# Kernel optimization log

Hardware: AMD Instinct MI355X
Metric: run time of the kernel (lower is better)

Reference implementation:

```python
import jax, jax.numpy as jnp
import numpy as np
from jax import lax

B, H, W, C = 4, 96, 96, 256
F = 256
KH = KW = 3
K = KH * KW
DG = 1
CG = C // DG
SH = SW = 1
DH = DW = 1
PAD_T = (DH * (KH - 1)) // 2  # 'same' padding (top/left) for 3x3 dil 1
PAD_L = (DW * (KW - 1)) // 2


def setup_inputs() -> dict:
    key = jax.random.key(0)
    k1, k2, k3 = jax.random.split(key, 3)
    x = jax.random.normal(k1, (B, H, W, C), jnp.float32)
    # offset/mask conv weights (orig init zeros; small random to exercise sampling)
    om_kernel = jax.random.normal(k2, (KH, KW, C, DG * 3 * K), jnp.float32) * 0.01
    om_bias = jnp.zeros((DG * 3 * K,), jnp.float32)
    stdv = 1.0 / np.sqrt(C * KH * KW)
    kernel = jax.random.uniform(k3, (K * C, F), jnp.float32, -stdv, stdv)
    bias = jnp.zeros((F,), jnp.float32)
    return {"x": x, "om_kernel": om_kernel, "om_bias": om_bias, "kernel": kernel, "bias": bias}


def reference(x, om_kernel, om_bias, kernel, bias):
    Bx, Hx, Wx, Cx = x.shape
    # offset/mask prediction conv (NHWC, 'SAME', matches keras Conv2D)
    om = lax.conv_general_dilated(
        x, om_kernel, (SH, SW), "SAME", rhs_dilation=(DH, DW),
        dimension_numbers=("NHWC", "HWIO", "NHWC")) + om_bias
    Ho, Wo = om.shape[1], om.shape[2]
    off = om[..., : 2 * DG * K].reshape(Bx, Ho, Wo, DG, K, 2)  # (dy, dx) per group/kpoint
    mask = jax.nn.sigmoid(om[..., 2 * DG * K :]).reshape(Bx, Ho, Wo, DG, K) * 2.0

    # base sampling grid: y = ho*SH - PAD_T + ki*DH (+ dy), similarly x
    base_y = (jnp.arange(Ho) * SH - PAD_T)[:, None] + (jnp.arange(KH) * DH)[None, :]  # [Ho,KH]
    base_x = (jnp.arange(Wo) * SW - PAD_L)[:, None] + (jnp.arange(KW) * DW)[None, :]  # [Wo,KW]
    gy = jnp.broadcast_to(base_y[:, None, :, None], (Ho, Wo, KH, KW)).reshape(Ho, Wo, K)
    gx = jnp.broadcast_to(base_x[None, :, None, :], (Ho, Wo, KH, KW)).reshape(Ho, Wo, K)

    py = gy[None, :, :, None, :].astype(x.dtype) + off[..., 0]  # [B,Ho,Wo,DG,K]
    px = gx[None, :, :, None, :].astype(x.dtype) + off[..., 1]

    # reorder to [B, N, DG] with N = Ho*Wo*K (K varies fastest after spatial)
    N = Ho * Wo * K
    py = py.transpose(0, 1, 2, 4, 3).reshape(Bx, N, DG)
    px = px.transpose(0, 1, 2, 4, 3).reshape(Bx, N, DG)
    mask_t = mask.transpose(0, 1, 2, 4, 3).reshape(Bx, N, DG)

    y0 = jnp.floor(py)
    x0 = jnp.floor(px)
    fy = py - y0
    fx = px - x0

    xf = x.reshape(Bx, Hx * Wx, DG, CG)
    val = jnp.zeros((Bx, N, DG, CG), x.dtype)
    for yi, wy in ((y0, 1.0 - fy), (y0 + 1.0, fy)):
        for xi, wx in ((x0, 1.0 - fx), (x0 + 1.0, fx)):
            valid = (yi >= 0) & (yi < Hx) & (xi >= 0) & (xi < Wx)
            yc = jnp.clip(yi, 0, Hx - 1).astype(jnp.int32)
            xc = jnp.clip(xi, 0, Wx - 1).astype(jnp.int32)
            lin = yc * Wx + xc  # [B,N,DG]
            g = jnp.take_along_axis(xf, lin[..., None], axis=1)  # [B,N,DG,CG]
            val = val + g * (wy * wx * valid.astype(x.dtype))[..., None]

    # modulate and im2col -> GEMM
    cols = (val * mask_t[..., None]).reshape(Bx, Ho * Wo, K * Cx)
    out = jnp.matmul(cols, kernel).reshape(Bx, Ho, Wo, -1) + bias
    return out
```

## Files before the change

### kernel.cpp

```cpp
#include <hip/hip_runtime.h>
#include <hip/hip_bf16.h>
#include <stdint.h>
#include <stddef.h>


namespace {
constexpr int H  = 96, W = 96, C = 256, F = 256;
constexpr int HP = 98;
constexpr int NP = 4 * 96 * 96;
constexpr int KC = 9 * 256;
}

typedef __attribute__((ext_vector_type(8))) short bf16x8;
typedef __attribute__((ext_vector_type(4))) float floatx4;

__device__ __forceinline__ void load_lds16(const void* g, void* l) {
  __builtin_amdgcn_global_load_lds((const __attribute__((address_space(1))) void*)g,
                                   (__attribute__((address_space(3))) void*)l,
                                   16, 0, 0);
}

__device__ __forceinline__ unsigned short bf16bits(float f) {
  __hip_bfloat16 h = __float2bfloat16(f);
  return *reinterpret_cast<unsigned short*>(&h);
}

__global__ __launch_bounds__(256) void k_pad(const float* __restrict__ x,
                                             uint2* __restrict__ xp) {
  const int tid = threadIdx.x;
  const int sub = tid >> 6, c4 = tid & 63;
  const int pp  = blockIdx.x * 4 + sub;
  const int b   = pp / (HP * HP);
  const int r   = pp % (HP * HP);
  const int y   = r / HP, xq = r % HP;
  uint2 o = {0u, 0u};
  if (y >= 1 && y <= H && xq >= 1 && xq <= W) {
    const float4 v = *(const float4*)(x + ((size_t)((b * H + (y - 1)) * W + (xq - 1))) * C + c4 * 4);
    o.x = (uint32_t)bf16bits(v.x) | ((uint32_t)bf16bits(v.y) << 16);
    o.y = (uint32_t)bf16bits(v.z) | ((uint32_t)bf16bits(v.w) << 16);
  }
  xp[(size_t)pp * 64 + c4] = o;
}

__global__ __launch_bounds__(256) void k_omw(const float* __restrict__ omk,
                                             __hip_bfloat16* __restrict__ wom) {
  const int kk = blockIdx.x;
  const int oc = blockIdx.y;
  const int c  = threadIdx.x;
  float v = (oc < 27) ? omk[(size_t)(kk * 256 + c) * 27 + oc] : 0.f;
  wom[(size_t)oc * KC + kk * 256 + c] = __float2bfloat16(v);
}

__global__ __launch_bounds__(256) void k_wt(const float* __restrict__ kern,
                                            __hip_bfloat16* __restrict__ wt) {
  __shared__ float t[64][65];
  const int kc0 = blockIdx.x * 64, f0 = blockIdx.y * 64;
  const int rr = threadIdx.x >> 6, cc = threadIdx.x & 63;
#pragma unroll
  for (int i = 0; i < 16; ++i) {
    const int row = rr * 16 + i;
    t[row][cc] = kern[(size_t)(kc0 + row) * F + f0 + cc];
  }
  __syncthreads();
#pragma unroll
  for (int i = 0; i < 16; ++i) {
    const int frow = rr * 16 + i;
    wt[(size_t)(f0 + frow) * KC + kc0 + cc] = __float2bfloat16(t[cc][frow]);
  }
}

__global__ __launch_bounds__(256) void k_omgemm(const __hip_bfloat16* __restrict__ xp,
                                                const __hip_bfloat16* __restrict__ wom,
                                                float* __restrict__ pOm) {
  __shared__ __align__(16) char lds[10240];
  const int tid  = threadIdx.x;
  const int m0   = blockIdx.x * 128;
  const int s    = blockIdx.y;
  const int lane = tid & 63, wave = tid >> 6;
  const int quad = lane >> 4, l16 = lane & 15;

  const int kp = tid & 3;
  const __hip_bfloat16* abase[2];
#pragma unroll
  for (int j = 0; j < 2; ++j) {
    const int row = (tid >> 2) + j * 64;
    const int p = m0 + row;
    const int b = p / (H * W);
    const int hw = p % (H * W);
    const int h = hw / W, w = hw % W;
    abase[j] = (const __hip_bfloat16*)xp + ((size_t)(b * HP + h) * HP + w) * C + kp * 8;
  }
  const __hip_bfloat16* bbase = wom + (size_t)(tid >> 2) * KC + kp * 8;

  floatx4 acc[2][2];
#pragma unroll
  for (int i = 0; i < 2; ++i)
#pragma unroll
    for (int j = 0; j < 2; ++j) acc[i][j] = (floatx4){0.f, 0.f, 0.f, 0.f};

  const int kbeg = s * 384;
#pragma unroll 1
  for (int k0 = kbeg; k0 < kbeg + 384; k0 += 32) {
    const int kk = k0 >> 8;
    const int c0 = k0 & 255;
    const int kh = kk / 3, kw = kk % 3;
    const int aoff = (kh * HP + kw) * C + c0;

    __syncthreads();
    load_lds16(abase[0] + aoff, &lds[tid * 16]);
    load_lds16(abase[1] + aoff, &lds[4096 + tid * 16]);
    if (tid < 128) load_lds16(bbase + k0, &lds[8192 + tid * 16]);
    __syncthreads();

    bf16x8 af[2], bfr[2];
#pragma unroll
    for (int mt = 0; mt < 2; ++mt)
      af[mt] = *(const bf16x8*)&lds[((wave * 32 + mt * 16 + l16) * 32 + quad * 8) * 2];
#pragma unroll
    for (int nt = 0; nt < 2; ++nt)
      bfr[nt] = *(const bf16x8*)&lds[8192 + ((nt * 16 + l16) * 32 + quad * 8) * 2];
#pragma unroll
    for (int mt = 0; mt < 2; ++mt)
#pragma unroll
      for (int nt = 0; nt < 2; ++nt)
        acc[mt][nt] = __builtin_amdgcn_mfma_f32_16x16x32_bf16(af[mt], bfr[nt], acc[mt][nt], 0, 0, 0);
  }

#pragma unroll
  for (int mt = 0; mt < 2; ++mt)
#pragma unroll
    for (int nt = 0; nt < 2; ++nt) {
      const int gm = m0 + wave * 32 + mt * 16 + quad * 4;
      const int gn = nt * 16 + l16;
#pragma unroll
      for (int r = 0; r < 4; ++r)
        __hip_atomic_fetch_add(&pOm[(size_t)(gm + r) * 32 + gn], acc[mt][nt][r],
                               __ATOMIC_RELAXED, __HIP_MEMORY_SCOPE_AGENT);
    }
}

__global__ __launch_bounds__(256) void k_sample(const uint2* __restrict__ xp,
                                                const float* __restrict__ pOm,
                                                const float* __restrict__ om_bias,
                                                uint2* __restrict__ cols) {
  const int tid = threadIdx.x;
  const int sub = tid >> 6, cid = tid & 63;
  const int p   = blockIdx.x * 4 + sub;
  const int b   = p / (H * W);
  const int hw  = p % (H * W);
  const int h = hw / W, w = hw % W;

  __shared__ float s_py[4][9], s_px[4][9], s_m[4][9];
  if (cid < 9) {
    const int k = cid;
    const float dy = om_bias[2 * k]     + pOm[(size_t)p * 32 + 2 * k];
    const float dx = om_bias[2 * k + 1] + pOm[(size_t)p * 32 + 2 * k + 1];
    const float mv = om_bias[18 + k]    + pOm[(size_t)p * 32 + 18 + k];
    s_py[sub][k] = (float)(h - 1 + k / 3) + dy;
    s_px[sub][k] = (float)(w - 1 + k % 3) + dx;
    s_m[sub][k]  = 2.f / (1.f + __expf(-mv));
  }
  __syncthreads();

  const uint2* __restrict__ xb = xp + (size_t)b * (HP * HP * 64) + cid;
  uint2* __restrict__ ob = cols + (size_t)p * (KC / 4) + cid;

#pragma unroll 1
  for (int k = 0; k < 9; ++k) {
    const float py = s_py[sub][k], px = s_px[sub][k], m = s_m[sub][k];
    const float y0f = floorf(py), x0f = floorf(px);
    const float fy = py - y0f, fx = px - x0f;
    const int y0 = (int)y0f, x0 = (int)x0f;
    float v0 = 0.f, v1 = 0.f, v2 = 0.f, v3 = 0.f;
#pragma unroll
    for (int dy2 = 0; dy2 < 2; ++dy2) {
#pragma unroll
      for (int dx2 = 0; dx2 < 2; ++dx2) {
        const int yi = y0 + dy2, xi = x0 + dx2;
        const bool valid = (yi >= 0) & (yi < H) & (xi >= 0) & (xi < W);
        const float wgt = valid ? (dy2 ? fy : 1.f - fy) * (dx2 ? fx : 1.f - fx) : 0.f;
        const int yc = min(max(yi + 1, 0), HP - 1);
        const int xc = min(max(xi + 1, 0), HP - 1);
        const uint2 v = xb[(size_t)(yc * HP + xc) * 64];
        v0 += wgt * __uint_as_float(v.x << 16);
        v1 += wgt * __uint_as_float(v.x & 0xffff0000u);
        v2 += wgt * __uint_as_float(v.y << 16);
        v3 += wgt * __uint_as_float(v.y & 0xffff0000u);
      }
    }
    uint2 o;
    o.x = (uint32_t)bf16bits(v0 * m) | ((uint32_t)bf16bits(v1 * m) << 16);
    o.y = (uint32_t)bf16bits(v2 * m) | ((uint32_t)bf16bits(v3 * m) << 16);
    ob[k * 64] = o;
  }
}

__global__ __launch_bounds__(256) void k_gemm(const __hip_bfloat16* __restrict__ A,
                                              const __hip_bfloat16* __restrict__ Bt,
                                              const float* __restrict__ bias,
                                              float* __restrict__ out) {
  __shared__ __align__(16) char lds[14336];

  const int tid  = threadIdx.x;
  const int m0   = blockIdx.x * 96;
  const int n0   = blockIdx.y * 128;
  const int lane = tid & 63, wave = tid >> 6;
  const int wm = wave & 1, wn = wave >> 1;
  const int quad = lane >> 4, l16 = lane & 15;

  floatx4 acc[3][4];
#pragma unroll
  for (int i = 0; i < 3; ++i)
#pragma unroll
    for (int j = 0; j < 4; ++j) acc[i][j] = (floatx4){0.f, 0.f, 0.f, 0.f};

#pragma unroll 1
  for (int k0 = 0; k0 < KC; k0 += 32) {
    __syncthreads();
    {
      const int row = tid >> 2, kp = tid & 3;
      load_lds16(A + (size_t)(m0 + row) * KC + k0 + kp * 8, &lds[tid * 16]);
      if (tid < 128)
        load_lds16(A + (size_t)(m0 + 64 + row) * KC + k0 + kp * 8, &lds[4096 + tid * 16]);
      load_lds16(Bt + (size_t)(n0 + row) * KC + k0 + kp * 8, &lds[6144 + tid * 16]);
      load_lds16(Bt + (size_t)(n0 + 64 + row) * KC + k0 + kp * 8, &lds[10240 + tid * 16]);
    }
    __syncthreads();

    bf16x8 af[3], bfr[4];
#pragma unroll
    for (int mt = 0; mt < 3; ++mt)
      af[mt] = *(const bf16x8*)&lds[((wm * 48 + mt * 16 + l16) * 32 + quad * 8) * 2];
#pragma unroll
    for (int nt = 0; nt < 4; ++nt)
      bfr[nt] = *(const bf16x8*)&lds[6144 + ((wn * 64 + nt * 16 + l16) * 32 + quad * 8) * 2];
#pragma unroll
    for (int mt = 0; mt < 3; ++mt)
#pragma unroll
      for (int nt = 0; nt < 4; ++nt)
        acc[mt][nt] = __builtin_amdgcn_mfma_f32_16x16x32_bf16(af[mt], bfr[nt], acc[mt][nt], 0, 0, 0);
  }

#pragma unroll
  for (int mt = 0; mt < 3; ++mt) {
#pragma unroll
    for (int nt = 0; nt < 4; ++nt) {
      const int gm = m0 + wm * 48 + mt * 16 + quad * 4;
      const int gn = n0 + wn * 64 + nt * 16 + l16;
      const float bs = bias[gn];
#pragma unroll
      for (int r = 0; r < 4; ++r)
        out[(size_t)(gm + r) * F + gn] = acc[mt][nt][r] + bs;
    }
  }
}

extern "C" void kernel_launch(void* const* d_in, const int* in_sizes, int n_in,
                              void* d_out, int out_size, void* d_ws, size_t ws_size,
                              hipStream_t stream) {
  const float* x    = (const float*)d_in[0];
  const float* omk  = (const float*)d_in[1];
  const float* omb  = (const float*)d_in[2];
  const float* kern = (const float*)d_in[3];
  const float* bias = (const float*)d_in[4];
  float* out = (float*)d_out;

  char* ws = (char*)d_ws;
  size_t off = 0;
  __hip_bfloat16* wt   = (__hip_bfloat16*)(ws + off); off += (size_t)F * KC * 2;
  __hip_bfloat16* xp   = (__hip_bfloat16*)(ws + off); off += (size_t)4 * HP * HP * C * 2;
  __hip_bfloat16* wom  = (__hip_bfloat16*)(ws + off); off += (size_t)32 * KC * 2;
  float*          pOm  = (float*)(ws + off);          off += (size_t)NP * 32 * 4;
  __hip_bfloat16* cols = (__hip_bfloat16*)(ws + off);

  k_pad   <<<dim3(4 * HP * HP / 4), 256, 0, stream>>>(x, (uint2*)xp);
  k_omw   <<<dim3(9, 32),           256, 0, stream>>>(omk, wom);
  k_wt    <<<dim3(KC / 64, F / 64), 256, 0, stream>>>(kern, wt);
  hipMemsetAsync(pOm, 0, (size_t)NP * 32 * 4, stream);
  k_omgemm<<<dim3(NP / 128, 6),     256, 0, stream>>>(xp, wom, pOm);
  k_sample<<<dim3(NP / 4),          256, 0, stream>>>((const uint2*)xp, pOm, omb, (uint2*)cols);
  k_gemm  <<<dim3(NP / 96, F / 128), 256, 0, stream>>>(cols, wt, bias, out);
}
```

Baseline: 250.5 us.

## Fuse deformable bilinear sampling into the GEMM A-tile load

Merges the sampling kernel and the GEMM into one kernel. Each block precomputes the per-pixel, per-kernel-point corner offsets and mask-scaled bilinear weights in LDS, then builds the bf16 A tile on the fly from the padded input for every K step. This removes the write and re-read of the large im2col cols buffer and one launch. In exchange, sampling is repeated for each of the two N-tile blocks, the gathers sit on the GEMM's critical path with no overlap, and the larger LDS footprint plus launch_bounds(256,3) may limit occupancy.

```diff
diff --git a/kernel.cpp b/kernel.cpp
--- a/kernel.cpp
+++ b/kernel.cpp
@@ -139,74 +139,52 @@
     }
 }
 
-__global__ __launch_bounds__(256) void k_sample(const uint2* __restrict__ xp,
-                                                const float* __restrict__ pOm,
-                                                const float* __restrict__ om_bias,
-                                                uint2* __restrict__ cols) {
-  const int tid = threadIdx.x;
-  const int sub = tid >> 6, cid = tid & 63;
-  const int p   = blockIdx.x * 4 + sub;
-  const int b   = p / (H * W);
-  const int hw  = p % (H * W);
-  const int h = hw / W, w = hw % W;
-
-  __shared__ float s_py[4][9], s_px[4][9], s_m[4][9];
-  if (cid < 9) {
-    const int k = cid;
+__global__ __launch_bounds__(256, 3) void k_fused(const uint2* __restrict__ xpu,
+                                                  const float* __restrict__ pOm,
+                                                  const float* __restrict__ om_bias,
+                                                  const __hip_bfloat16* __restrict__ Bt,
+                                                  const float* __restrict__ bias,
+                                                  float* __restrict__ out) {
+  __shared__ __align__(16) char s_a[6144];
+  __shared__ __align__(16) char s_b[8192];
+  __shared__ __align__(16) float s_ow[96 * 9 * 8];
+
+  const int tid  = threadIdx.x;
+  const int m0   = blockIdx.x * 96;
+  const int n0   = blockIdx.y * 128;
+  const int b    = m0 / (H * W);
+  const int h    = (m0 % (H * W)) / W;
+  const int lane = tid & 63, wave = tid >> 6;
+  const int wm = wave & 1, wn = wave >> 1;
+  const int quad = lane >> 4, l16 = lane & 15;
+
+#pragma unroll 1
+  for (int i = tid; i < 96 * 9; i += 256) {
+    const int wq = i % 96, k = i / 96;
+    const int p  = m0 + wq;
     const float dy = om_bias[2 * k]     + pOm[(size_t)p * 32 + 2 * k];
     const float dx = om_bias[2 * k + 1] + pOm[(size_t)p * 32 + 2 * k + 1];
     const float mv = om_bias[18 + k]    + pOm[(size_t)p * 32 + 18 + k];
-    s_py[sub][k] = (float)(h - 1 + k / 3) + dy;
-    s_px[sub][k] = (float)(w - 1 + k % 3) + dx;
-    s_m[sub][k]  = 2.f / (1.f + __expf(-mv));
-  }
-  __syncthreads();
-
-  const uint2* __restrict__ xb = xp + (size_t)b * (HP * HP * 64) + cid;
-  uint2* __restrict__ ob = cols + (size_t)p * (KC / 4) + cid;
-
-#pragma unroll 1
-  for (int k = 0; k < 9; ++k) {
-    const float py = s_py[sub][k], px = s_px[sub][k], m = s_m[sub][k];
-    const float y0f = floorf(py), x0f = floorf(px);
-    const float fy = py - y0f, fx = px - x0f;
+    const float m  = 2.f / (1.f + __expf(-mv));
+    const float sy = (float)(h - 1 + k / 3) + dy;
+    const float sx = (float)(wq - 1 + k % 3) + dx;
+    const float y0f = floorf(sy), x0f = floorf(sx);
+    const float fy = sy - y0f, fx = sx - x0f;
     const int y0 = (int)y0f, x0 = (int)x0f;
-    float v0 = 0.f, v1 = 0.f, v2 = 0.f, v3 = 0.f;
-#pragma unroll
-    for (int dy2 = 0; dy2 < 2; ++dy2) {
-#pragma unroll
-      for (int dx2 = 0; dx2 < 2; ++dx2) {
-        const int yi = y0 + dy2, xi = x0 + dx2;
-        const bool valid = (yi >= 0) & (yi < H) & (xi >= 0) & (xi < W);
-        const float wgt = valid ? (dy2 ? fy : 1.f - fy) * (dx2 ? fx : 1.f - fx) : 0.f;
-        const int yc = min(max(yi + 1, 0), HP - 1);
-        const int xc = min(max(xi + 1, 0), HP - 1);
-        const uint2 v = xb[(size_t)(yc * HP + xc) * 64];
-        v0 += wgt * __uint_as_float(v.x << 16);
-        v1 += wgt * __uint_as_float(v.x & 0xffff0000u);
-        v2 += wgt * __uint_as_float(v.y << 16);
-        v3 += wgt * __uint_as_float(v.y & 0xffff0000u);
-      }
-    }
-    uint2 o;
-    o.x = (uint32_t)bf16bits(v0 * m) | ((uint32_t)bf16bits(v1 * m) << 16);
-    o.y = (uint32_t)bf16bits(v2 * m) | ((uint32_t)bf16bits(v3 * m) << 16);
-    ob[k * 64] = o;
-  }
-}
-
-__global__ __launch_bounds__(256) void k_gemm(const __hip_bfloat16* __restrict__ A,
-                                              const __hip_bfloat16* __restrict__ Bt,
-                                              const float* __restrict__ bias,
-                                              float* __restrict__ out) {
-  __shared__ __align__(16) char lds[14336];
-
-  const int tid  = threadIdx.x;
-  const int m0   = blockIdx.x * 96;
-  const int n0   = blockIdx.y * 128;
-  const int lane = tid & 63, wave = tid >> 6;
-  const int wm = wave & 1, wn = wave >> 1;
-  const int quad = lane >> 4, l16 = lane & 15;
+    float* ow = &s_ow[(size_t)(wq * 9 + k) * 8];
+#pragma unroll
+    for (int c2 = 0; c2 < 4; ++c2) {
+      const int dy2 = c2 >> 1, dx2 = c2 & 1;
+      const int yi = y0 + dy2, xi = x0 + dx2;
+      const bool valid = (yi >= 0) & (yi < H) & (xi >= 0) & (xi < W);
+      const float wgt = valid ? (dy2 ? fy : 1.f - fy) * (dx2 ? fx : 1.f - fx) * m : 0.f;
+      const int yc = min(max(yi + 1, 0), HP - 1);
+      const int xc = min(max(xi + 1, 0), HP - 1);
+      const int off = ((b * HP + yc) * HP + xc) * 64;
+      ow[c2 * 2]     = __int_as_float(off);
+      ow[c2 * 2 + 1] = wgt;
+    }
+  }
 
   floatx4 acc[3][4];
 #pragma unroll
@@ -216,24 +194,60 @@
 
 #pragma unroll 1
   for (int k0 = 0; k0 < KC; k0 += 32) {
+    const int kk = k0 >> 8;
+    const int cb = (k0 & 255) >> 2;
+
     __syncthreads();
     {
       const int row = tid >> 2, kp = tid & 3;
-      load_lds16(A + (size_t)(m0 + row) * KC + k0 + kp * 8, &lds[tid * 16]);
-      if (tid < 128)
-        load_lds16(A + (size_t)(m0 + 64 + row) * KC + k0 + kp * 8, &lds[4096 + tid * 16]);
-      load_lds16(Bt + (size_t)(n0 + row) * KC + k0 + kp * 8, &lds[6144 + tid * 16]);
-      load_lds16(Bt + (size_t)(n0 + 64 + row) * KC + k0 + kp * 8, &lds[10240 + tid * 16]);
+      load_lds16(Bt + (size_t)(n0 + row)      * KC + k0 + kp * 8, &s_b[tid * 16]);
+      load_lds16(Bt + (size_t)(n0 + 64 + row) * KC + k0 + kp * 8, &s_b[4096 + tid * 16]);
+    }
+#pragma unroll
+    for (int u = 0; u < 3; ++u) {
+      const int id  = tid + u * 256;
+      const int pxl = id >> 3, g = id & 7;
+      const float4* owp = (const float4*)&s_ow[(size_t)(pxl * 9 + kk) * 8];
+      const float4 ow0 = owp[0], ow1 = owp[1];
+      float v0 = 0.f, v1 = 0.f, v2 = 0.f, v3 = 0.f;
+      {
+        const uint2 v = xpu[(size_t)__float_as_int(ow0.x) + cb + g];
+        const float wg = ow0.y;
+        v0 += wg * __uint_as_float(v.x << 16); v1 += wg * __uint_as_float(v.x & 0xffff0000u);
+        v2 += wg * __uint_as_float(v.y << 16); v3 += wg * __uint_as_float(v.y & 0xffff0000u);
+      }
+      {
+        const uint2 v = xpu[(size_t)__float_as_int(ow0.z) + cb + g];
+        const float wg = ow0.w;
+        v0 += wg * __uint_as_float(v.x << 16); v1 += wg * __uint_as_float(v.x & 0xffff0000u);
+        v2 += wg * __uint_as_float(v.y << 16); v3 += wg * __uint_as_float(v.y & 0xffff0000u);
+      }
+      {
+        const uint2 v = xpu[(size_t)__float_as_int(ow1.x) + cb + g];
+        const float wg = ow1.y;
+        v0 += wg * __uint_as_float(v.x << 16); v1 += wg * __uint_as_float(v.x & 0xffff0000u);
+        v2 += wg * __uint_as_float(v.y << 16); v3 += wg * __uint_as_float(v.y & 0xffff0000u);
+      }
+      {
+        const uint2 v = xpu[(size_t)__float_as_int(ow1.z) + cb + g];
+        const float wg = ow1.w;
+        v0 += wg * __uint_as_float(v.x << 16); v1 += wg * __uint_as_float(v.x & 0xffff0000u);
+        v2 += wg * __uint_as_float(v.y << 16); v3 += wg * __uint_as_float(v.y & 0xffff0000u);
+      }
+      uint2 o;
+      o.x = (uint32_t)bf16bits(v0) | ((uint32_t)bf16bits(v1) << 16);
+      o.y = (uint32_t)bf16bits(v2) | ((uint32_t)bf16bits(v3) << 16);
+      *(uint2*)&s_a[pxl * 64 + g * 8] = o;
     }
     __syncthreads();
 
     bf16x8 af[3], bfr[4];
 #pragma unroll
     for (int mt = 0; mt < 3; ++mt)
-      af[mt] = *(const bf16x8*)&lds[((wm * 48 + mt * 16 + l16) * 32 + quad * 8) * 2];
+      af[mt] = *(const bf16x8*)&s_a[((wm * 48 + mt * 16 + l16) * 32 + quad * 8) * 2];
 #pragma unroll
     for (int nt = 0; nt < 4; ++nt)
-      bfr[nt] = *(const bf16x8*)&lds[6144 + ((wn * 64 + nt * 16 + l16) * 32 + quad * 8) * 2];
+      bfr[nt] = *(const bf16x8*)&s_b[((wn * 64 + nt * 16 + l16) * 32 + quad * 8) * 2];
 #pragma unroll
     for (int mt = 0; mt < 3; ++mt)
 #pragma unroll
@@ -271,13 +285,11 @@
   __hip_bfloat16* xp   = (__hip_bfloat16*)(ws + off); off += (size_t)4 * HP * HP * C * 2;
   __hip_bfloat16* wom  = (__hip_bfloat16*)(ws + off); off += (size_t)32 * KC * 2;
   float*          pOm  = (float*)(ws + off);          off += (size_t)NP * 32 * 4;
-  __hip_bfloat16* cols = (__hip_bfloat16*)(ws + off);
 
   k_pad   <<<dim3(4 * HP * HP / 4), 256, 0, stream>>>(x, (uint2*)xp);
   k_omw   <<<dim3(9, 32),           256, 0, stream>>>(omk, wom);
   k_wt    <<<dim3(KC / 64, F / 64), 256, 0, stream>>>(kern, wt);
   hipMemsetAsync(pOm, 0, (size_t)NP * 32 * 4, stream);
   k_omgemm<<<dim3(NP / 128, 6),     256, 0, stream>>>(xp, wom, pOm);
-  k_sample<<<dim3(NP / 4),          256, 0, stream>>>((const uint2*)xp, pOm, omb, (uint2*)cols);
-  k_gemm  <<<dim3(NP / 96, F / 128), 256, 0, stream>>>(cols, wt, bias, out);
-}
+  k_fused <<<dim3(NP / 96, F / 128), 256, 0, stream>>>((const uint2*)xp, pOm, omb, wt, bias, out);
+}
```

Measured after the change: 283.7 us. 1.13x slower.

## Merge prep kernels and memset into one launch; widen sampling to 16-byte loads

Applied to the files above, without the earlier changes.

Pad/convert, offset-weight conversion, main-weight transpose and the pOm zeroing are folded into one k_prep kernel that branches on block index, replacing three launches plus a memset. The sampling kernel now handles 8 pixels per block with 32 threads each doing 16-byte (8 bf16) loads and stores. Per-tap bilinear offsets and mask-folded weights are precomputed once into shared memory instead of being recomputed per thread. This cuts launch overhead and per-thread address arithmetic, at the cost of branch-divergent block roles in the fused prep kernel.

```diff
diff --git a/kernel.cpp b/kernel.cpp
--- a/kernel.cpp
+++ b/kernel.cpp
@@ -9,6 +9,11 @@
 constexpr int HP = 98;
 constexpr int NP = 4 * 96 * 96;
 constexpr int KC = 9 * 256;
+
+constexpr int NB_PAD  = 4 * HP * HP / 8;
+constexpr int NB_OMW  = 9 * 32;
+constexpr int NB_WT   = (KC / 64) * (F / 64);
+constexpr int NB_ZERO = NP * 32 * 4 / 4096;
 }
 
 typedef __attribute__((ext_vector_type(8))) short bf16x8;
@@ -20,52 +25,64 @@
                                    16, 0, 0);
 }
 
-__device__ __forceinline__ unsigned short bf16bits(float f) {
-  __hip_bfloat16 h = __float2bfloat16(f);
-  return *reinterpret_cast<unsigned short*>(&h);
-}
-
-__global__ __launch_bounds__(256) void k_pad(const float* __restrict__ x,
-                                             uint2* __restrict__ xp) {
-  const int tid = threadIdx.x;
-  const int sub = tid >> 6, c4 = tid & 63;
-  const int pp  = blockIdx.x * 4 + sub;
-  const int b   = pp / (HP * HP);
-  const int r   = pp % (HP * HP);
-  const int y   = r / HP, xq = r % HP;
-  uint2 o = {0u, 0u};
-  if (y >= 1 && y <= H && xq >= 1 && xq <= W) {
-    const float4 v = *(const float4*)(x + ((size_t)((b * H + (y - 1)) * W + (xq - 1))) * C + c4 * 4);
-    o.x = (uint32_t)bf16bits(v.x) | ((uint32_t)bf16bits(v.y) << 16);
-    o.y = (uint32_t)bf16bits(v.z) | ((uint32_t)bf16bits(v.w) << 16);
-  }
-  xp[(size_t)pp * 64 + c4] = o;
-}
-
-__global__ __launch_bounds__(256) void k_omw(const float* __restrict__ omk,
-                                             __hip_bfloat16* __restrict__ wom) {
-  const int kk = blockIdx.x;
-  const int oc = blockIdx.y;
-  const int c  = threadIdx.x;
-  float v = (oc < 27) ? omk[(size_t)(kk * 256 + c) * 27 + oc] : 0.f;
-  wom[(size_t)oc * KC + kk * 256 + c] = __float2bfloat16(v);
-}
-
-__global__ __launch_bounds__(256) void k_wt(const float* __restrict__ kern,
-                                            __hip_bfloat16* __restrict__ wt) {
+__device__ __forceinline__ uint32_t pk2(float lo, float hi) {
+  __hip_bfloat162 t = __float22bfloat162_rn(float2{lo, hi});
+  return *reinterpret_cast<uint32_t*>(&t);
+}
+
+__device__ __forceinline__ void acc8(uint4 v, float w, float* a) {
+  a[0] += w * __uint_as_float(v.x << 16); a[1] += w * __uint_as_float(v.x & 0xffff0000u);
+  a[2] += w * __uint_as_float(v.y << 16); a[3] += w * __uint_as_float(v.y & 0xffff0000u);
+  a[4] += w * __uint_as_float(v.z << 16); a[5] += w * __uint_as_float(v.z & 0xffff0000u);
+  a[6] += w * __uint_as_float(v.w << 16); a[7] += w * __uint_as_float(v.w & 0xffff0000u);
+}
+
+__global__ __launch_bounds__(256) void k_prep(const float* __restrict__ x,
+                                              const float* __restrict__ omk,
+                                              const float* __restrict__ kern,
+                                              uint4* __restrict__ xp4,
+                                              __hip_bfloat16* __restrict__ wom,
+                                              __hip_bfloat16* __restrict__ wt,
+                                              float4* __restrict__ pOmz) {
   __shared__ float t[64][65];
-  const int kc0 = blockIdx.x * 64, f0 = blockIdx.y * 64;
-  const int rr = threadIdx.x >> 6, cc = threadIdx.x & 63;
-#pragma unroll
-  for (int i = 0; i < 16; ++i) {
-    const int row = rr * 16 + i;
-    t[row][cc] = kern[(size_t)(kc0 + row) * F + f0 + cc];
-  }
-  __syncthreads();
-#pragma unroll
-  for (int i = 0; i < 16; ++i) {
-    const int frow = rr * 16 + i;
-    wt[(size_t)(f0 + frow) * KC + kc0 + cc] = __float2bfloat16(t[cc][frow]);
+  const int bi = blockIdx.x, tid = threadIdx.x;
+
+  if (bi < NB_PAD) {
+    const int sub = tid >> 5, cid = tid & 31;
+    const int pp  = bi * 8 + sub;
+    const int b   = pp / (HP * HP);
+    const int r   = pp % (HP * HP);
+    const int y   = r / HP, xq = r % HP;
+    uint4 o = {0u, 0u, 0u, 0u};
+    if (y >= 1 && y <= H && xq >= 1 && xq <= W) {
+      const float* src = x + ((size_t)((b * H + (y - 1)) * W + (xq - 1))) * C + cid * 8;
+      const float4 v0 = *(const float4*)src;
+      const float4 v1 = *(const float4*)(src + 4);
+      o.x = pk2(v0.x, v0.y); o.y = pk2(v0.z, v0.w);
+      o.z = pk2(v1.x, v1.y); o.w = pk2(v1.z, v1.w);
+    }
+    xp4[(size_t)pp * 32 + cid] = o;
+  } else if (bi < NB_PAD + NB_OMW) {
+    const int i  = bi - NB_PAD;
+    const int kk = i / 32, oc = i % 32;
+    float v = (oc < 27) ? omk[(size_t)(kk * 256 + tid) * 27 + oc] : 0.f;
+    wom[(size_t)oc * KC + kk * 256 + tid] = __float2bfloat16(v);
+  } else if (bi < NB_PAD + NB_OMW + NB_WT) {
+    const int j   = bi - NB_PAD - NB_OMW;
+    const int kc0 = (j % (KC / 64)) * 64, f0 = (j / (KC / 64)) * 64;
+    const int rr = tid >> 6, cc = tid & 63;
+#pragma unroll
+    for (int i = 0; i < 16; ++i)
+      t[rr * 16 + i][cc] = kern[(size_t)(kc0 + rr * 16 + i) * F + f0 + cc];
+    __syncthreads();
+#pragma unroll
+    for (int i = 0; i < 16; ++i) {
+      const int frow = rr * 16 + i;
+      wt[(size_t)(f0 + frow) * KC + kc0 + cc] = __float2bfloat16(t[cc][frow]);
+    }
+  } else {
+    const int j = bi - NB_PAD - NB_OMW - NB_WT;
+    pOmz[(size_t)j * 256 + tid] = (float4){0.f, 0.f, 0.f, 0.f};
   }
 }
 
@@ -88,7 +105,7 @@
     const int b = p / (H * W);
     const int hw = p % (H * W);
     const int h = hw / W, w = hw % W;
-    abase[j] = (const __hip_bfloat16*)xp + ((size_t)(b * HP + h) * HP + w) * C + kp * 8;
+    abase[j] = xp + ((size_t)(b * HP + h) * HP + w) * C + kp * 8;
   }
   const __hip_bfloat16* bbase = wom + (size_t)(tid >> 2) * KC + kp * 8;
 
@@ -139,59 +156,60 @@
     }
 }
 
-__global__ __launch_bounds__(256) void k_sample(const uint2* __restrict__ xp,
+__global__ __launch_bounds__(256) void k_sample(const uint4* __restrict__ xp4,
                                                 const float* __restrict__ pOm,
                                                 const float* __restrict__ om_bias,
-                                                uint2* __restrict__ cols) {
+                                                uint4* __restrict__ cols4) {
+  __shared__ float2 s_ow[8][9][4];
+
   const int tid = threadIdx.x;
-  const int sub = tid >> 6, cid = tid & 63;
-  const int p   = blockIdx.x * 4 + sub;
-  const int b   = p / (H * W);
-  const int hw  = p % (H * W);
-  const int h = hw / W, w = hw % W;
-
-  __shared__ float s_py[4][9], s_px[4][9], s_m[4][9];
-  if (cid < 9) {
-    const int k = cid;
+  const int sub = tid >> 5, cid = tid & 31;
+
+  if (tid < 72) {
+    const int ps = tid / 9, k = tid % 9;
+    const int p  = blockIdx.x * 8 + ps;
+    const int b  = p / (H * W);
+    const int hw = p % (H * W);
+    const int h = hw / W, w = hw % W;
     const float dy = om_bias[2 * k]     + pOm[(size_t)p * 32 + 2 * k];
     const float dx = om_bias[2 * k + 1] + pOm[(size_t)p * 32 + 2 * k + 1];
     const float mv = om_bias[18 + k]    + pOm[(size_t)p * 32 + 18 + k];
-    s_py[sub][k] = (float)(h - 1 + k / 3) + dy;
-    s_px[sub][k] = (float)(w - 1 + k % 3) + dx;
-    s_m[sub][k]  = 2.f / (1.f + __expf(-mv));
+    const float m  = 2.f / (1.f + __expf(-mv));
+    const float sy = (float)(h - 1 + k / 3) + dy;
+    const float sx = (float)(w - 1 + k % 3) + dx;
+    const float y0f = floorf(sy), x0f = floorf(sx);
+    const float fy = sy - y0f, fx = sx - x0f;
+    const int y0 = (int)y0f, x0 = (int)x0f;
+#pragma unroll
+    for (int c2 = 0; c2 < 4; ++c2) {
+      const int dy2 = c2 >> 1, dx2 = c2 & 1;
+      const int yi = y0 + dy2, xi = x0 + dx2;
+      const bool valid = (yi >= 0) & (yi < H) & (xi >= 0) & (xi < W);
+      const float wgt = valid ? (dy2 ? fy : 1.f - fy) * (dx2 ? fx : 1.f - fx) * m : 0.f;
+      const int yc = min(max(yi + 1, 0), HP - 1);
+      const int xc = min(max(xi + 1, 0), HP - 1);
+      const int off = ((b * HP + yc) * HP + xc) * 32;
+      s_ow[ps][k][c2] = float2{__int_as_float(off), wgt};
+    }
   }
   __syncthreads();
 
-  const uint2* __restrict__ xb = xp + (size_t)b * (HP * HP * 64) + cid;
-  uint2* __restrict__ ob = cols + (size_t)p * (KC / 4) + cid;
+  const int p = blockIdx.x * 8 + sub;
+  uint4* __restrict__ ob = cols4 + (size_t)p * 288 + cid;
 
 #pragma unroll 1
   for (int k = 0; k < 9; ++k) {
-    const float py = s_py[sub][k], px = s_px[sub][k], m = s_m[sub][k];
-    const float y0f = floorf(py), x0f = floorf(px);
-    const float fy = py - y0f, fx = px - x0f;
-    const int y0 = (int)y0f, x0 = (int)x0f;
-    float v0 = 0.f, v1 = 0.f, v2 = 0.f, v3 = 0.f;
-#pragma unroll
-    for (int dy2 = 0; dy2 < 2; ++dy2) {
-#pragma unroll
-      for (int dx2 = 0; dx2 < 2; ++dx2) {
-        const int yi = y0 + dy2, xi = x0 + dx2;
-        const bool valid = (yi >= 0) & (yi < H) & (xi >= 0) & (xi < W);
-        const float wgt = valid ? (dy2 ? fy : 1.f - fy) * (dx2 ? fx : 1.f - fx) : 0.f;
-        const int yc = min(max(yi + 1, 0), HP - 1);
-        const int xc = min(max(xi + 1, 0), HP - 1);
-        const uint2 v = xb[(size_t)(yc * HP + xc) * 64];
-        v0 += wgt * __uint_as_float(v.x << 16);
-        v1 += wgt * __uint_as_float(v.x & 0xffff0000u);
-        v2 += wgt * __uint_as_float(v.y << 16);
-        v3 += wgt * __uint_as_float(v.y & 0xffff0000u);
-      }
-    }
-    uint2 o;
-    o.x = (uint32_t)bf16bits(v0 * m) | ((uint32_t)bf16bits(v1 * m) << 16);
-    o.y = (uint32_t)bf16bits(v2 * m) | ((uint32_t)bf16bits(v3 * m) << 16);
-    ob[k * 64] = o;
+    const float2 ow0 = s_ow[sub][k][0], ow1 = s_ow[sub][k][1];
+    const float2 ow2 = s_ow[sub][k][2], ow3 = s_ow[sub][k][3];
+    float a[8] = {0.f, 0.f, 0.f, 0.f, 0.f, 0.f, 0.f, 0.f};
+    acc8(xp4[(size_t)__float_as_int(ow0.x) + cid], ow0.y, a);
+    acc8(xp4[(size_t)__float_as_int(ow1.x) + cid], ow1.y, a);
+    acc8(xp4[(size_t)__float_as_int(ow2.x) + cid], ow2.y, a);
+    acc8(xp4[(size_t)__float_as_int(ow3.x) + cid], ow3.y, a);
+    uint4 o;
+    o.x = pk2(a[0], a[1]); o.y = pk2(a[2], a[3]);
+    o.z = pk2(a[4], a[5]); o.w = pk2(a[6], a[7]);
+    ob[k * 32] = o;
   }
 }
 
@@ -273,11 +291,9 @@
   float*          pOm  = (float*)(ws + off);          off += (size_t)NP * 32 * 4;
   __hip_bfloat16* cols = (__hip_bfloat16*)(ws + off);
 
-  k_pad   <<<dim3(4 * HP * HP / 4), 256, 0, stream>>>(x, (uint2*)xp);
-  k_omw   <<<dim3(9, 32),           256, 0, stream>>>(omk, wom);
-  k_wt    <<<dim3(KC / 64, F / 64), 256, 0, stream>>>(kern, wt);
-  hipMemsetAsync(pOm, 0, (size_t)NP * 32 * 4, stream);
-  k_omgemm<<<dim3(NP / 128, 6),     256, 0, stream>>>(xp, wom, pOm);
-  k_sample<<<dim3(NP / 4),          256, 0, stream>>>((const uint2*)xp, pOm, omb, (uint2*)cols);
+  k_prep  <<<dim3(NB_PAD + NB_OMW + NB_WT + NB_ZERO), 256, 0, stream>>>(
+      x, omk, kern, (uint4*)xp, wom, wt, (float4*)pOm);
+  k_omgemm<<<dim3(NP / 128, 6),      256, 0, stream>>>(xp, wom, pOm);
+  k_sample<<<dim3(NP / 8),           256, 0, stream>>>((const uint4*)xp, pOm, omb, (uint4*)cols);
   k_gemm  <<<dim3(NP / 96, F / 128), 256, 0, stream>>>(cols, wt, bias, out);
 }
```

Measured after the change: 227.5 us. 1.1x faster.
